# Kernel optimization log

Hardware: AMD Instinct MI355X
Metric: run time of the kernel (lower is better)

Reference implementation:

```python
import jax, jax.numpy as jnp
import numpy as np


def _excl_cumsum(f, axis, reverse):
    """Exclusive (strict) cumulative sum along `axis`, optionally from the far end."""
    if reverse:
        c = jnp.flip(jnp.cumsum(jnp.flip(f, axis), axis=axis), axis)
    else:
        c = jnp.cumsum(f, axis=axis)
    return c - f  # inclusive minus self = exclusive (strict inequality)


def _dir_sum(f, direction):
    """Strict directional 2D prefix sum over [B,T,H,W].
    NE: sum over h' < h (north) and w' > w (east).
    SW: sum over h' > h and w' < w.
    SE: sum over h' > h and w' > w.
    """
    rev_h, rev_w = {"NE": (False, True), "SW": (True, False), "SE": (True, True)}[direction]
    return _excl_cumsum(_excl_cumsum(f, 2, rev_h), 3, rev_w)


def _weight(alpha, x):
    # per-tree, per-channel linear weighting contracted over channels: [T,C],[B,C,H,W] -> [B,T,H,W]
    return jnp.einsum("tc,bchw->bthw", alpha, x)


def setup_inputs() -> dict:
    key = jax.random.key(0)
    ks = jax.random.split(key, 7)
    B, C, H, W = 16, 32, 256, 256
    T2 = 8  # num_trees // 2
    return {
        "x": jax.random.normal(ks[0], (B, C, H, W), dtype=jnp.float32),
        "alpha_1": jax.random.normal(ks[1], (T2, C), dtype=jnp.float32),
        "alpha_2": jax.random.normal(ks[2], (T2, C), dtype=jnp.float32),
        "alpha_3": jax.random.normal(ks[3], (T2, C), dtype=jnp.float32),
        "alpha_1p": jax.random.normal(ks[4], (T2, C), dtype=jnp.float32),
        "alpha_2p": jax.random.normal(ks[5], (T2, C), dtype=jnp.float32),
        "alpha_3p": jax.random.normal(ks[6], (T2, C), dtype=jnp.float32),
    }


def reference(x, alpha_1, alpha_2, alpha_3, alpha_1p, alpha_2p, alpha_3p):
    # Linear tree: root(alpha_1) --NE--> node(alpha_2) --SW--> leaf(alpha_3)
    v3 = _weight(alpha_3, x)
    v2 = _weight(alpha_2, x) * _dir_sum(v3, "SW")
    linear = _weight(alpha_1, x) * _dir_sum(v2, "NE")
    # Cherry tree: root(alpha_1p) with children SW->leaf(alpha_3p), SE->leaf(alpha_2p)
    cherry = (
        _weight(alpha_1p, x)
        * _dir_sum(_weight(alpha_3p, x), "SW")
        * _dir_sum(_weight(alpha_2p, x), "SE")
    )
    # cat=True: concatenate the two tree families along the tree/channel axis
    return jnp.concatenate([linear, cherry], axis=1)  # [B, num_trees, H, W]
```

## Files before the change

kernel.cpp:

```cpp
#include <hip/hip_runtime.h>

#define B   16
#define C   32
#define T2  8
#define H   256
#define W   256
#define NF  (B * T2 * H * W)
#define NCH 8
#define CH  32
#define SUMSZ (B * T2 * NCH * W)


__device__ __forceinline__ float wave_incl_scan(float s, int lane) {
#pragma unroll
  for (int d = 1; d < 64; d <<= 1) {
    float n = __shfl_up(s, (unsigned)d, 64);
    if (lane >= d) s += n;
  }
  return s;
}

__global__ __launch_bounds__(256) void k_weight6(
    const float* __restrict__ x,
    const float* __restrict__ a1,  const float* __restrict__ a2,
    const float* __restrict__ a3,  const float* __restrict__ a1p,
    const float* __restrict__ a2p, const float* __restrict__ a3p,
    float* __restrict__ ws, float* __restrict__ out) {
  int pix = blockIdx.x * 256 + threadIdx.x;
  int b  = pix >> 16;
  int hw = pix & 65535;
  const float* xb = x + (size_t)(b * C) * 65536 + hw;

  float acc1[T2] = {}, acc2[T2] = {}, acc3[T2] = {};
  float acc1p[T2] = {}, acc2p[T2] = {}, acc3p[T2] = {};

#pragma unroll
  for (int c = 0; c < C; ++c) {
    float xv = xb[(size_t)c * 65536];
#pragma unroll
    for (int t = 0; t < T2; ++t) {
      acc3[t]  = fmaf(a3 [t * C + c], xv, acc3[t]);
      acc2[t]  = fmaf(a2 [t * C + c], xv, acc2[t]);
      acc1[t]  = fmaf(a1 [t * C + c], xv, acc1[t]);
      acc3p[t] = fmaf(a3p[t * C + c], xv, acc3p[t]);
      acc2p[t] = fmaf(a2p[t * C + c], xv, acc2p[t]);
      acc1p[t] = fmaf(a1p[t * C + c], xv, acc1p[t]);
    }
  }

#pragma unroll
  for (int t = 0; t < T2; ++t) {
    size_t so = ((size_t)(b * T2 + t) << 16) + hw;
    ws[so]               = acc3[t];
    ws[(size_t)NF + so]  = acc2[t];
    ws[2ull * NF + so]   = acc3p[t];
    ws[3ull * NF + so]   = acc2p[t];
    out[((size_t)(b * 16 + t)     << 16) + hw] = acc1[t];
    out[((size_t)(b * 16 + 8 + t) << 16) + hw] = acc1p[t];
  }
}

__global__ __launch_bounds__(256) void k_chunksums(float* __restrict__ ws) {
  int f    = blockIdx.x >> 10;
  int bid  = blockIdx.x & 1023;
  int slice = bid >> 3, chunk = bid & 7;
  int w = threadIdx.x;
  const size_t fieldOff[3] = {0, 2ull * NF, 3ull * NF};
  const float* base = ws + fieldOff[f] + ((size_t)slice << 16) + (size_t)(chunk * CH) * W + w;
  float s = 0.f;
#pragma unroll
  for (int h = 0; h < CH; ++h) s += base[h * W];
  float* sums = ws + 4ull * NF + (size_t)f * SUMSZ;
  sums[(size_t)(slice * NCH + chunk) * W + w] = s;
}

__global__ __launch_bounds__(256) void k_linear_mid(float* __restrict__ ws) {
  __shared__ float tile[CH][W];
  __shared__ float colpart[4][W];
  int slice = blockIdx.x >> 3, chunk = blockIdx.x & 7;
  int tid = threadIdx.x, lane = tid & 63, wv = tid >> 6;

  const float* S3 = ws + 4ull * NF;
  float* Sv2      = ws + 4ull * NF + 3ull * SUMSZ;
  float* fbase  = ws + ((size_t)slice << 16) + (size_t)(chunk * CH) * W;
  const float* f2base = ws + (size_t)NF + ((size_t)slice << 16) + (size_t)(chunk * CH) * W;

  {
    int w = tid;
    float run = 0.f;
#pragma unroll
    for (int c = 0; c < NCH; ++c)
      if (c > chunk) run += S3[(size_t)(slice * NCH + c) * W + w];
#pragma unroll
    for (int h = CH - 1; h >= 0; --h) {
      float v = fbase[(size_t)h * W + w];
      tile[h][w] = run;
      run += v;
    }
  }
  __syncthreads();

  float4 cs = {0.f, 0.f, 0.f, 0.f};
#pragma unroll
  for (int i = 0; i < 8; ++i) {
    int h = wv * 8 + i;
    float4 a = *(const float4*)&tile[h][lane * 4];
    float s = a.x + a.y + a.z + a.w;
    float incl = wave_incl_scan(s, lane);
    float excl = incl - s;
    float e0 = excl, e1 = e0 + a.x, e2 = e1 + a.y, e3 = e2 + a.z;
    float4 f = *(const float4*)&f2base[(size_t)h * W + lane * 4];
    float4 o;
    o.x = f.x * e0; o.y = f.y * e1; o.z = f.z * e2; o.w = f.w * e3;
    *(float4*)&fbase[(size_t)h * W + lane * 4] = o;
    cs.x += o.x; cs.y += o.y; cs.z += o.z; cs.w += o.w;
  }
  *(float4*)&colpart[wv][lane * 4] = cs;
  __syncthreads();
  {
    int w = tid;
    float sv = colpart[0][w] + colpart[1][w] + colpart[2][w] + colpart[3][w];
    Sv2[(size_t)(slice * NCH + chunk) * W + w] = sv;
  }
}

__global__ __launch_bounds__(256) void k_linear_fin(const float* __restrict__ ws,
                                                    float* __restrict__ out) {
  __shared__ float tile[CH][W];
  int slice = blockIdx.x >> 3, chunk = blockIdx.x & 7;
  int tid = threadIdx.x, lane = tid & 63, wv = tid >> 6;

  const float* Sv2 = ws + 4ull * NF + 3ull * SUMSZ;
  const float* vbase = ws + ((size_t)slice << 16) + (size_t)(chunk * CH) * W;

  {
    int w = tid;
    float run = 0.f;
#pragma unroll
    for (int c = 0; c < NCH; ++c)
      if (c < chunk) run += Sv2[(size_t)(slice * NCH + c) * W + w];
#pragma unroll
    for (int h = 0; h < CH; ++h) {
      float v = vbase[(size_t)h * W + w];
      tile[h][w] = run;
      run += v;
    }
  }
  __syncthreads();

  int b = slice >> 3, t = slice & 7;
  float* obase = out + ((size_t)(b * 16 + t) << 16) + (size_t)(chunk * CH) * W;
#pragma unroll
  for (int i = 0; i < 8; ++i) {
    int h = wv * 8 + i;
    float4 a = *(const float4*)&tile[h][lane * 4];
    float s = a.x + a.y + a.z + a.w;
    float incl = wave_incl_scan(s, lane);
    float excl = incl - s;
    float total = __shfl(incl, 63, 64);
    float r0 = total - excl - a.x;
    float r1 = r0 - a.y, r2 = r1 - a.z, r3 = r2 - a.w;
    float4 f = *(const float4*)&obase[(size_t)h * W + lane * 4];
    float4 o;
    o.x = f.x * r0; o.y = f.y * r1; o.z = f.z * r2; o.w = f.w * r3;
    *(float4*)&obase[(size_t)h * W + lane * 4] = o;
  }
}

__global__ __launch_bounds__(256) void k_cherry2(const float* __restrict__ ws,
                                                 float* __restrict__ out) {
  __shared__ float tA[CH][W];
  __shared__ float tB[CH][W];
  int slice = blockIdx.x >> 3, chunk = blockIdx.x & 7;
  int tid = threadIdx.x, lane = tid & 63, wv = tid >> 6;

  const float* S3p = ws + 4ull * NF + 1ull * SUMSZ;
  const float* S2p = ws + 4ull * NF + 2ull * SUMSZ;
  const float* abase = ws + 2ull * NF + ((size_t)slice << 16) + (size_t)(chunk * CH) * W;
  const float* bbase = ws + 3ull * NF + ((size_t)slice << 16) + (size_t)(chunk * CH) * W;

  {
    int w = tid;
    float runA = 0.f, runB = 0.f;
#pragma unroll
    for (int c = 0; c < NCH; ++c)
      if (c > chunk) {
        runA += S3p[(size_t)(slice * NCH + c) * W + w];
        runB += S2p[(size_t)(slice * NCH + c) * W + w];
      }
#pragma unroll
    for (int h = CH - 1; h >= 0; --h) {
      float va = abase[(size_t)h * W + w];
      float vb = bbase[(size_t)h * W + w];
      tA[h][w] = runA; runA += va;
      tB[h][w] = runB; runB += vb;
    }
  }
  __syncthreads();

  int b = slice >> 3, t = slice & 7;
  float* obase = out + ((size_t)(b * 16 + 8 + t) << 16) + (size_t)(chunk * CH) * W;
#pragma unroll
  for (int i = 0; i < 8; ++i) {
    int h = wv * 8 + i;
    float4 a = *(const float4*)&tA[h][lane * 4];
    float4 bq = *(const float4*)&tB[h][lane * 4];
    float sa = a.x + a.y + a.z + a.w;
    float sb = bq.x + bq.y + bq.z + bq.w;
    float ia = wave_incl_scan(sa, lane);
    float ib = wave_incl_scan(sb, lane);
    float ea = ia - sa;
    float eb = ib - sb;
    float tb = __shfl(ib, 63, 64);
    float fa0 = ea, fa1 = fa0 + a.x, fa2 = fa1 + a.y, fa3 = fa2 + a.z;
    float rb0 = tb - eb - bq.x;
    float rb1 = rb0 - bq.y, rb2 = rb1 - bq.z, rb3 = rb2 - bq.w;
    float4 f = *(const float4*)&obase[(size_t)h * W + lane * 4];
    float4 o;
    o.x = f.x * fa0 * rb0;
    o.y = f.y * fa1 * rb1;
    o.z = f.z * fa2 * rb2;
    o.w = f.w * fa3 * rb3;
    *(float4*)&obase[(size_t)h * W + lane * 4] = o;
  }
}

__global__ __launch_bounds__(256) void k_weight3(
    const float* __restrict__ x,
    const float* __restrict__ aA, const float* __restrict__ aB,
    const float* __restrict__ aC,
    float* __restrict__ ws0, float* __restrict__ ws1,
    float* __restrict__ out, int outoff) {
  int pix = blockIdx.x * 256 + threadIdx.x;
  int b  = pix >> 16;
  int hw = pix & 65535;
  const float* xb = x + (size_t)(b * C) * 65536 + hw;
  float accA[T2] = {}, accB[T2] = {}, accC[T2] = {};
#pragma unroll
  for (int c = 0; c < C; ++c) {
    float xv = xb[(size_t)c * 65536];
#pragma unroll
    for (int t = 0; t < T2; ++t) {
      accA[t] = fmaf(aA[t * C + c], xv, accA[t]);
      accB[t] = fmaf(aB[t * C + c], xv, accB[t]);
      accC[t] = fmaf(aC[t * C + c], xv, accC[t]);
    }
  }
#pragma unroll
  for (int t = 0; t < T2; ++t) {
    size_t so = ((size_t)(b * T2 + t) << 16) + hw;
    ws0[so] = accB[t];
    ws1[so] = accC[t];
    out[((size_t)(b * 16 + outoff + t) << 16) + hw] = accA[t];
  }
}

__global__ __launch_bounds__(256) void k_colscan_rev(float* __restrict__ base_) {
  float* base = base_ + ((size_t)blockIdx.x << 16) + threadIdx.x;
  float run = 0.f;
#pragma unroll 8
  for (int h = 255; h >= 0; --h) {
    float v = base[h << 8];
    base[h << 8] = run;
    run += v;
  }
}

__global__ __launch_bounds__(256) void k_colscan_fwd(float* __restrict__ base_) {
  float* base = base_ + ((size_t)blockIdx.x << 16) + threadIdx.x;
  float run = 0.f;
#pragma unroll 8
  for (int h = 0; h < 256; ++h) {
    float v = base[h << 8];
    base[h << 8] = run;
    run += v;
  }
}

__global__ __launch_bounds__(256) void k_row_v2(float* __restrict__ wsA,
                                                const float* __restrict__ wsB) {
  int lane = threadIdx.x & 63;
  int r = blockIdx.x * 4 + (threadIdx.x >> 6);
  float4* arow = (float4*)(wsA + (size_t)r * 256);
  const float4* brow = (const float4*)(wsB + (size_t)r * 256);
  float4 a = arow[lane];
  float s = a.x + a.y + a.z + a.w;
  float incl = wave_incl_scan(s, lane);
  float excl = incl - s;
  float e0 = excl, e1 = e0 + a.x, e2 = e1 + a.y, e3 = e2 + a.z;
  float4 bq = brow[lane];
  float4 o;
  o.x = bq.x * e0; o.y = bq.y * e1; o.z = bq.z * e2; o.w = bq.w * e3;
  arow[lane] = o;
}

__global__ __launch_bounds__(256) void k_final_linear(const float* __restrict__ wsV,
                                                      float* __restrict__ out) {
  int lane = threadIdx.x & 63;
  int r = blockIdx.x * 4 + (threadIdx.x >> 6);
  const float4* vrow = (const float4*)(wsV + (size_t)r * 256);
  float4 a = vrow[lane];
  float s = a.x + a.y + a.z + a.w;
  float incl = wave_incl_scan(s, lane);
  float excl = incl - s;
  float total = __shfl(incl, 63, 64);
  float r0 = total - excl - a.x;
  float r1 = r0 - a.y, r2 = r1 - a.z, r3 = r2 - a.w;
  int b = r >> 11, t = (r >> 8) & 7, h = r & 255;
  float* orow = out + ((size_t)((b * 16 + t) * 256 + h)) * 256;
  float4 f = ((const float4*)orow)[lane];
  float4 o;
  o.x = f.x * r0; o.y = f.y * r1; o.z = f.z * r2; o.w = f.w * r3;
  ((float4*)orow)[lane] = o;
}

__global__ __launch_bounds__(256) void k_cherry(const float* __restrict__ wsAp,
                                                const float* __restrict__ wsBp,
                                                float* __restrict__ out) {
  int lane = threadIdx.x & 63;
  int r = blockIdx.x * 4 + (threadIdx.x >> 6);
  const float4* ap = (const float4*)(wsAp + (size_t)r * 256);
  const float4* bp = (const float4*)(wsBp + (size_t)r * 256);
  float4 a  = ap[lane];
  float4 bq = bp[lane];
  float sa = a.x + a.y + a.z + a.w;
  float sb = bq.x + bq.y + bq.z + bq.w;
  float ia = wave_incl_scan(sa, lane);
  float ib = wave_incl_scan(sb, lane);
  float ea = ia - sa;
  float eb = ib - sb;
  float tb = __shfl(ib, 63, 64);
  float fa0 = ea, fa1 = fa0 + a.x, fa2 = fa1 + a.y, fa3 = fa2 + a.z;
  float rb0 = tb - eb - bq.x;
  float rb1 = rb0 - bq.y, rb2 = rb1 - bq.z, rb3 = rb2 - bq.w;
  int b = r >> 11, t = (r >> 8) & 7, h = r & 255;
  float* orow = out + ((size_t)((b * 16 + 8 + t) * 256 + h)) * 256;
  float4 f = ((const float4*)orow)[lane];
  float4 o;
  o.x = f.x * fa0 * rb0;
  o.y = f.y * fa1 * rb1;
  o.z = f.z * fa2 * rb2;
  o.w = f.w * fa3 * rb3;
  ((float4*)orow)[lane] = o;
}

extern "C" void kernel_launch(void* const* d_in, const int* in_sizes, int n_in,
                              void* d_out, int out_size, void* d_ws, size_t ws_size,
                              hipStream_t stream) {
  const float* x   = (const float*)d_in[0];
  const float* a1  = (const float*)d_in[1];
  const float* a2  = (const float*)d_in[2];
  const float* a3  = (const float*)d_in[3];
  const float* a1p = (const float*)d_in[4];
  const float* a2p = (const float*)d_in[5];
  const float* a3p = (const float*)d_in[6];
  float* out = (float*)d_out;
  float* ws  = (float*)d_ws;

  const size_t field_bytes = (size_t)NF * 4;
  const size_t need_fast2  = 4 * field_bytes + 4ull * SUMSZ * 4;

  if (ws_size >= need_fast2) {
    k_weight6<<<4096, 256, 0, stream>>>(x, a1, a2, a3, a1p, a2p, a3p, ws, out);
    k_chunksums<<<3072, 256, 0, stream>>>(ws);
    k_linear_mid<<<1024, 256, 0, stream>>>(ws);
    k_linear_fin<<<1024, 256, 0, stream>>>(ws, out);
    k_cherry2<<<1024, 256, 0, stream>>>(ws, out);
  } else if (ws_size >= 4 * field_bytes) {
    k_weight6<<<4096, 256, 0, stream>>>(x, a1, a2, a3, a1p, a2p, a3p, ws, out);
    k_colscan_rev<<<128, 256, 0, stream>>>(ws);
    k_colscan_rev<<<256, 256, 0, stream>>>(ws + 2ull * NF);
    k_row_v2<<<8192, 256, 0, stream>>>(ws, ws + NF);
    k_colscan_fwd<<<128, 256, 0, stream>>>(ws);
    k_final_linear<<<8192, 256, 0, stream>>>(ws, out);
    k_cherry<<<8192, 256, 0, stream>>>(ws + 2ull * NF, ws + 3ull * NF, out);
  } else {
    float* ws0 = ws;
    float* ws1 = ws + NF;
    k_weight3<<<4096, 256, 0, stream>>>(x, a1, a3, a2, ws0, ws1, out, 0);
    k_colscan_rev<<<128, 256, 0, stream>>>(ws0);
    k_row_v2<<<8192, 256, 0, stream>>>(ws0, ws1);
    k_colscan_fwd<<<128, 256, 0, stream>>>(ws0);
    k_final_linear<<<8192, 256, 0, stream>>>(ws0, out);
    k_weight3<<<4096, 256, 0, stream>>>(x, a1p, a3p, a2p, ws0, ws1, out, 8);
    k_colscan_rev<<<256, 256, 0, stream>>>(ws0);
    k_cherry<<<8192, 256, 0, stream>>>(ws0, ws1, out);
  }
}
```

Measured before the change: 338.7 us.

## Stage x in LDS for weighting, vectorize chunk sums, use 512-thread scan blocks

The weighting kernel now stages the 32 channel values of 256 pixels in shared memory and loops over trees one at a time. This keeps six accumulators instead of 48 live and so cuts register pressure. The chunk-sum kernel has each wavefront sum one chunk with float4 loads. The three scan kernels move to 512 threads: the column scan is split in two halves with a handoff through shared memory, and each wave handles four rows instead of eight. The aim is more parallelism and occupancy, at the cost of extra syncs and 32KB of LDS in the weighting kernel.

```diff
diff --git a/kernel.cpp b/kernel.cpp
--- a/kernel.cpp
+++ b/kernel.cpp
@@ -26,84 +26,104 @@
     const float* __restrict__ a3,  const float* __restrict__ a1p,
     const float* __restrict__ a2p, const float* __restrict__ a3p,
     float* __restrict__ ws, float* __restrict__ out) {
-  int pix = blockIdx.x * 256 + threadIdx.x;
-  int b  = pix >> 16;
-  int hw = pix & 65535;
-  const float* xb = x + (size_t)(b * C) * 65536 + hw;
-
-  float acc1[T2] = {}, acc2[T2] = {}, acc3[T2] = {};
-  float acc1p[T2] = {}, acc2p[T2] = {}, acc3p[T2] = {};
-
-#pragma unroll
-  for (int c = 0; c < C; ++c) {
-    float xv = xb[(size_t)c * 65536];
-#pragma unroll
-    for (int t = 0; t < T2; ++t) {
-      acc3[t]  = fmaf(a3 [t * C + c], xv, acc3[t]);
-      acc2[t]  = fmaf(a2 [t * C + c], xv, acc2[t]);
-      acc1[t]  = fmaf(a1 [t * C + c], xv, acc1[t]);
-      acc3p[t] = fmaf(a3p[t * C + c], xv, acc3p[t]);
-      acc2p[t] = fmaf(a2p[t * C + c], xv, acc2p[t]);
-      acc1p[t] = fmaf(a1p[t * C + c], xv, acc1p[t]);
-    }
-  }
-
-#pragma unroll
+  __shared__ float xs[C][W];
+  int tid = threadIdx.x;
+  int b   = blockIdx.x >> 8;
+  int hwb = (blockIdx.x & 255) << 8;
+  const float* xb = x + (((size_t)b * C) << 16) + hwb;
+
+#pragma unroll
+  for (int c = 0; c < C; ++c) xs[c][tid] = xb[((size_t)c << 16) + tid];
+  __syncthreads();
+
+#pragma unroll 1
   for (int t = 0; t < T2; ++t) {
-    size_t so = ((size_t)(b * T2 + t) << 16) + hw;
-    ws[so]               = acc3[t];
-    ws[(size_t)NF + so]  = acc2[t];
-    ws[2ull * NF + so]   = acc3p[t];
-    ws[3ull * NF + so]   = acc2p[t];
-    out[((size_t)(b * 16 + t)     << 16) + hw] = acc1[t];
-    out[((size_t)(b * 16 + 8 + t) << 16) + hw] = acc1p[t];
+    float s1 = 0.f, s2 = 0.f, s3 = 0.f, s1p = 0.f, s2p = 0.f, s3p = 0.f;
+#pragma unroll
+    for (int c = 0; c < C; ++c) {
+      float xv = xs[c][tid];
+      s1  = fmaf(a1 [t * C + c], xv, s1);
+      s2  = fmaf(a2 [t * C + c], xv, s2);
+      s3  = fmaf(a3 [t * C + c], xv, s3);
+      s1p = fmaf(a1p[t * C + c], xv, s1p);
+      s2p = fmaf(a2p[t * C + c], xv, s2p);
+      s3p = fmaf(a3p[t * C + c], xv, s3p);
+    }
+    size_t so = (((size_t)(b * T2 + t)) << 16) + hwb + tid;
+    ws[so]               = s3;
+    ws[(size_t)NF + so]  = s2;
+    ws[2ull * NF + so]   = s3p;
+    ws[3ull * NF + so]   = s2p;
+    out[(((size_t)(b * 16 + t))     << 16) + hwb + tid] = s1;
+    out[(((size_t)(b * 16 + 8 + t)) << 16) + hwb + tid] = s1p;
   }
 }
 
 __global__ __launch_bounds__(256) void k_chunksums(float* __restrict__ ws) {
-  int f    = blockIdx.x >> 10;
-  int bid  = blockIdx.x & 1023;
-  int slice = bid >> 3, chunk = bid & 7;
-  int w = threadIdx.x;
-  const size_t fieldOff[3] = {0, 2ull * NF, 3ull * NF};
-  const float* base = ws + fieldOff[f] + ((size_t)slice << 16) + (size_t)(chunk * CH) * W + w;
-  float s = 0.f;
-#pragma unroll
-  for (int h = 0; h < CH; ++h) s += base[h * W];
+  int unit = blockIdx.x * 4 + (threadIdx.x >> 6);
+  int lane = threadIdx.x & 63;
+  int f = unit >> 10;
+  int r = unit & 1023;
+  int slice = r >> 3, chunk = r & 7;
+  size_t foff = (f == 0) ? 0 : ((f == 1) ? 2ull * NF : 3ull * NF);
+  const float* base = ws + foff + ((size_t)slice << 16) +
+                      (size_t)(chunk * CH) * W + lane * 4;
+  float4 s = {0.f, 0.f, 0.f, 0.f};
+#pragma unroll
+  for (int h = 0; h < CH; ++h) {
+    float4 v = *(const float4*)(base + (size_t)h * W);
+    s.x += v.x; s.y += v.y; s.z += v.z; s.w += v.w;
+  }
   float* sums = ws + 4ull * NF + (size_t)f * SUMSZ;
-  sums[(size_t)(slice * NCH + chunk) * W + w] = s;
-}
-
-__global__ __launch_bounds__(256) void k_linear_mid(float* __restrict__ ws) {
+  *(float4*)(sums + (size_t)(slice * NCH + chunk) * W + lane * 4) = s;
+}
+
+__global__ __launch_bounds__(512) void k_linear_mid(float* __restrict__ ws) {
   __shared__ float tile[CH][W];
-  __shared__ float colpart[4][W];
+  __shared__ float colpart[8][W];
   int slice = blockIdx.x >> 3, chunk = blockIdx.x & 7;
-  int tid = threadIdx.x, lane = tid & 63, wv = tid >> 6;
+  int tid = threadIdx.x;
+  int col = tid & 255, half = tid >> 8;
 
   const float* S3 = ws + 4ull * NF;
   float* Sv2      = ws + 4ull * NF + 3ull * SUMSZ;
-  float* fbase  = ws + ((size_t)slice << 16) + (size_t)(chunk * CH) * W;
-  const float* f2base = ws + (size_t)NF + ((size_t)slice << 16) + (size_t)(chunk * CH) * W;
-
-  {
-    int w = tid;
+  float* fbase    = ws + ((size_t)slice << 16) + (size_t)(chunk * CH) * W;
+  const float* f2base = ws + (size_t)NF + ((size_t)slice << 16) +
+                        (size_t)(chunk * CH) * W;
+
+  float pre[16];
+  if (half == 1) {
+#pragma unroll
+    for (int h = 0; h < 16; ++h) pre[h] = fbase[(size_t)h * W + col];
+  } else {
     float run = 0.f;
 #pragma unroll
     for (int c = 0; c < NCH; ++c)
-      if (c > chunk) run += S3[(size_t)(slice * NCH + c) * W + w];
-#pragma unroll
-    for (int h = CH - 1; h >= 0; --h) {
-      float v = fbase[(size_t)h * W + w];
-      tile[h][w] = run;
+      if (c > chunk) run += S3[(size_t)(slice * NCH + c) * W + col];
+#pragma unroll
+    for (int h = CH - 1; h >= 16; --h) {
+      float v = fbase[(size_t)h * W + col];
+      tile[h][col] = run;
       run += v;
     }
-  }
-  __syncthreads();
-
+    colpart[0][col] = run;
+  }
+  __syncthreads();
+  if (half == 1) {
+    float run = colpart[0][col];
+#pragma unroll
+    for (int h = 15; h >= 0; --h) {
+      tile[h][col] = run;
+      run += pre[h];
+    }
+  }
+  __syncthreads();
+
+  int lane = tid & 63, wv = tid >> 6;
   float4 cs = {0.f, 0.f, 0.f, 0.f};
 #pragma unroll
-  for (int i = 0; i < 8; ++i) {
-    int h = wv * 8 + i;
+  for (int i = 0; i < 4; ++i) {
+    int h = wv * 4 + i;
     float4 a = *(const float4*)&tile[h][lane * 4];
     float s = a.x + a.y + a.z + a.w;
     float incl = wave_incl_scan(s, lane);
@@ -117,42 +137,59 @@
   }
   *(float4*)&colpart[wv][lane * 4] = cs;
   __syncthreads();
-  {
-    int w = tid;
-    float sv = colpart[0][w] + colpart[1][w] + colpart[2][w] + colpart[3][w];
-    Sv2[(size_t)(slice * NCH + chunk) * W + w] = sv;
-  }
-}
-
-__global__ __launch_bounds__(256) void k_linear_fin(const float* __restrict__ ws,
+  if (tid < 256) {
+    float sv = 0.f;
+#pragma unroll
+    for (int k = 0; k < 8; ++k) sv += colpart[k][col];
+    Sv2[(size_t)(slice * NCH + chunk) * W + col] = sv;
+  }
+}
+
+__global__ __launch_bounds__(512) void k_linear_fin(const float* __restrict__ ws,
                                                     float* __restrict__ out) {
   __shared__ float tile[CH][W];
+  __shared__ float handoff[W];
   int slice = blockIdx.x >> 3, chunk = blockIdx.x & 7;
-  int tid = threadIdx.x, lane = tid & 63, wv = tid >> 6;
+  int tid = threadIdx.x;
+  int col = tid & 255, half = tid >> 8;
 
   const float* Sv2 = ws + 4ull * NF + 3ull * SUMSZ;
   const float* vbase = ws + ((size_t)slice << 16) + (size_t)(chunk * CH) * W;
 
-  {
-    int w = tid;
+  float pre[16];
+  if (half == 1) {
+#pragma unroll
+    for (int h = 0; h < 16; ++h) pre[h] = vbase[(size_t)(h + 16) * W + col];
+  } else {
     float run = 0.f;
 #pragma unroll
     for (int c = 0; c < NCH; ++c)
-      if (c < chunk) run += Sv2[(size_t)(slice * NCH + c) * W + w];
-#pragma unroll
-    for (int h = 0; h < CH; ++h) {
-      float v = vbase[(size_t)h * W + w];
-      tile[h][w] = run;
+      if (c < chunk) run += Sv2[(size_t)(slice * NCH + c) * W + col];
+#pragma unroll
+    for (int h = 0; h < 16; ++h) {
+      float v = vbase[(size_t)h * W + col];
+      tile[h][col] = run;
       run += v;
     }
-  }
-  __syncthreads();
-
+    handoff[col] = run;
+  }
+  __syncthreads();
+  if (half == 1) {
+    float run = handoff[col];
+#pragma unroll
+    for (int h = 16; h < CH; ++h) {
+      tile[h][col] = run;
+      run += pre[h - 16];
+    }
+  }
+  __syncthreads();
+
+  int lane = tid & 63, wv = tid >> 6;
   int b = slice >> 3, t = slice & 7;
   float* obase = out + ((size_t)(b * 16 + t) << 16) + (size_t)(chunk * CH) * W;
 #pragma unroll
-  for (int i = 0; i < 8; ++i) {
-    int h = wv * 8 + i;
+  for (int i = 0; i < 4; ++i) {
+    int h = wv * 4 + i;
     float4 a = *(const float4*)&tile[h][lane * 4];
     float s = a.x + a.y + a.z + a.w;
     float incl = wave_incl_scan(s, lane);
@@ -167,12 +204,13 @@
   }
 }
 
-__global__ __launch_bounds__(256) void k_cherry2(const float* __restrict__ ws,
+__global__ __launch_bounds__(512) void k_cherry2(const float* __restrict__ ws,
                                                  float* __restrict__ out) {
   __shared__ float tA[CH][W];
   __shared__ float tB[CH][W];
   int slice = blockIdx.x >> 3, chunk = blockIdx.x & 7;
-  int tid = threadIdx.x, lane = tid & 63, wv = tid >> 6;
+  int tid = threadIdx.x;
+  int col = tid & 255, half = tid >> 8;
 
   const float* S3p = ws + 4ull * NF + 1ull * SUMSZ;
   const float* S2p = ws + 4ull * NF + 2ull * SUMSZ;
@@ -180,30 +218,29 @@
   const float* bbase = ws + 3ull * NF + ((size_t)slice << 16) + (size_t)(chunk * CH) * W;
 
   {
-    int w = tid;
-    float runA = 0.f, runB = 0.f;
+    const float* S    = (half == 0) ? S3p : S2p;
+    const float* base = (half == 0) ? abase : bbase;
+    float* tdst       = (half == 0) ? &tA[0][0] : &tB[0][0];
+    float run = 0.f;
 #pragma unroll
     for (int c = 0; c < NCH; ++c)
-      if (c > chunk) {
-        runA += S3p[(size_t)(slice * NCH + c) * W + w];
-        runB += S2p[(size_t)(slice * NCH + c) * W + w];
-      }
+      if (c > chunk) run += S[(size_t)(slice * NCH + c) * W + col];
 #pragma unroll
     for (int h = CH - 1; h >= 0; --h) {
-      float va = abase[(size_t)h * W + w];
-      float vb = bbase[(size_t)h * W + w];
-      tA[h][w] = runA; runA += va;
-      tB[h][w] = runB; runB += vb;
-    }
-  }
-  __syncthreads();
-
+      float v = base[(size_t)h * W + col];
+      tdst[h * W + col] = run;
+      run += v;
+    }
+  }
+  __syncthreads();
+
+  int lane = tid & 63, wv = tid >> 6;
   int b = slice >> 3, t = slice & 7;
   float* obase = out + ((size_t)(b * 16 + 8 + t) << 16) + (size_t)(chunk * CH) * W;
 #pragma unroll
-  for (int i = 0; i < 8; ++i) {
-    int h = wv * 8 + i;
-    float4 a = *(const float4*)&tA[h][lane * 4];
+  for (int i = 0; i < 4; ++i) {
+    int h = wv * 4 + i;
+    float4 a  = *(const float4*)&tA[h][lane * 4];
     float4 bq = *(const float4*)&tB[h][lane * 4];
     float sa = a.x + a.y + a.z + a.w;
     float sb = bq.x + bq.y + bq.z + bq.w;
@@ -362,10 +399,10 @@
 
   if (ws_size >= need_fast2) {
     k_weight6<<<4096, 256, 0, stream>>>(x, a1, a2, a3, a1p, a2p, a3p, ws, out);
-    k_chunksums<<<3072, 256, 0, stream>>>(ws);
-    k_linear_mid<<<1024, 256, 0, stream>>>(ws);
-    k_linear_fin<<<1024, 256, 0, stream>>>(ws, out);
-    k_cherry2<<<1024, 256, 0, stream>>>(ws, out);
+    k_chunksums<<<768, 256, 0, stream>>>(ws);
+    k_linear_mid<<<1024, 512, 0, stream>>>(ws);
+    k_linear_fin<<<1024, 512, 0, stream>>>(ws, out);
+    k_cherry2<<<1024, 512, 0, stream>>>(ws, out);
   } else if (ws_size >= 4 * field_bytes) {
     k_weight6<<<4096, 256, 0, stream>>>(x, a1, a2, a3, a1p, a2p, a3p, ws, out);
     k_colscan_rev<<<128, 256, 0, stream>>>(ws);
```

New measurement: 429.3 us. 26.8% more time.
